# Kernel optimization log

Measured on AMD Instinct MI355X. Metric: run time of the kernel, lower is better.

The kernel has to match this reference:

```python
import jax, jax.numpy as jnp
import numpy as np

H = 32

def setup_inputs() -> dict:
    key = jax.random.key(0)
    ks = jax.random.split(key, 8)
    B, S = 256, 4096
    scale = 1.0 / np.sqrt(H)
    return {
        "lstm_outputs": jax.random.normal(ks[0], (B, S, H), dtype=jnp.float32),
        "final_hidden": jax.random.normal(ks[1], (B, H), dtype=jnp.float32),
        "Wq": jax.random.uniform(ks[2], (H, H), jnp.float32, -scale, scale),
        "bq": jax.random.uniform(ks[3], (H,), jnp.float32, -scale, scale),
        "Wk": jax.random.uniform(ks[4], (H, H), jnp.float32, -scale, scale),
        "bk": jax.random.uniform(ks[5], (H,), jnp.float32, -scale, scale),
        "Wv": jax.random.uniform(ks[6], (H, 1), jnp.float32, -scale, scale),
        "bv": jax.random.uniform(ks[7], (1,), jnp.float32, -scale, scale),
    }

def reference(lstm_outputs, final_hidden, Wq, bq, Wk, bk, Wv, bv):
    # keys: [B,S,H], query: [B,H]
    keys = jnp.einsum('bsh,hd->bsd', lstm_outputs, Wk) + bk
    query = final_hidden @ Wq + bq
    tanhed = jnp.tanh(query[:, None, :] + keys)            # [B,S,H]
    scores = jnp.einsum('bsh,h->bs', tanhed, Wv[:, 0]) + bv[0]  # [B,S]
    att_weights = jax.nn.softmax(scores, axis=-1)          # [B,S]
    context = jnp.einsum('bs,bsh->bh', att_weights, keys)  # [B,H]
    return context, att_weights
```

## Files before the change

### kernel.cpp

```cpp
#include <hip/hip_runtime.h>
#include <math.h>

#define HD 32
#define BB 256
#define SS 4096
#define BLK 256
#define POSB 256
#define NCH (SS / POSB)
#define PAD 33
#define PSTRIDE 33

__device__ __forceinline__ float tanh_fast(float x) {
  float e = __builtin_amdgcn_exp2f(x * 2.8853900817779268f);
  return 1.0f - 2.0f * __builtin_amdgcn_rcpf(e + 1.0f);
}
__device__ __forceinline__ float exp_fast(float x) {
  return __builtin_amdgcn_exp2f(x * 1.4426950408889634f);
}

__global__ void __launch_bounds__(BLK, 4) bahdanau_p1(
    const float* __restrict__ lstm, const float* __restrict__ fh,
    const float* __restrict__ Wq, const float* __restrict__ bq,
    const float* __restrict__ Wk, const float* __restrict__ bk,
    const float* __restrict__ Wv, const float* __restrict__ bv,
    float* __restrict__ scores_out, float* __restrict__ partials) {
  __shared__ float sX[POSB * PAD];
  __shared__ float sWk[HD * HD];
  __shared__ float sE[POSB];
  __shared__ float sQB[HD];
  __shared__ float sWv[HD];
  __shared__ float sYp[8][HD];
  __shared__ float sRedL[BLK / 64];

  const int tid = threadIdx.x;
  const int b = blockIdx.x >> 4;
  const int chunk = blockIdx.x & (NCH - 1);
  const int base = chunk * POSB;
  const int lane = tid & 63, wid = tid >> 6;

  ((float4*)sWk)[tid] = ((const float4*)Wk)[tid];

  const float* gx = lstm + ((size_t)b * SS + base) * HD;
  float4 stg[8];
#pragma unroll
  for (int i = 0; i < 8; i++) stg[i] = ((const float4*)gx)[tid + i * BLK];

  if (tid < HD) {
    float acc = bq[tid] + bk[tid];
    const float* fhb = fh + b * HD;
#pragma unroll
    for (int j = 0; j < HD; j++) acc += fhb[j] * Wq[j * HD + tid];
    sQB[tid] = acc;
    sWv[tid] = Wv[tid];
  }

#pragma unroll
  for (int i = 0; i < 8; i++) {
    const int f = tid + i * BLK;
    const int pos = f >> 3, q = f & 7;
    float* d = &sX[pos * PAD + q * 4];
    d[0] = stg[i].x; d[1] = stg[i].y; d[2] = stg[i].z; d[3] = stg[i].w;
  }
  __syncthreads();

  const float* xr = &sX[tid * PAD];
  float acc[HD];
#pragma unroll
  for (int h = 0; h < HD; h++) acc[h] = 0.f;
#pragma unroll 2
  for (int j = 0; j < HD; j++) {
    const float xj = xr[j];
    const float4* wrow = (const float4*)&sWk[j * HD];
#pragma unroll
    for (int h4 = 0; h4 < 8; h4++) {
      const float4 w = wrow[h4];
      acc[4 * h4 + 0] = fmaf(xj, w.x, acc[4 * h4 + 0]);
      acc[4 * h4 + 1] = fmaf(xj, w.y, acc[4 * h4 + 1]);
      acc[4 * h4 + 2] = fmaf(xj, w.z, acc[4 * h4 + 2]);
      acc[4 * h4 + 3] = fmaf(xj, w.w, acc[4 * h4 + 3]);
    }
  }

  float sc = bv[0];
#pragma unroll
  for (int h4 = 0; h4 < 8; h4++) {
    const float4 qb = ((const float4*)sQB)[h4];
    const float4 wv = ((const float4*)sWv)[h4];
    sc = fmaf(tanh_fast(qb.x + acc[4 * h4 + 0]), wv.x, sc);
    sc = fmaf(tanh_fast(qb.y + acc[4 * h4 + 1]), wv.y, sc);
    sc = fmaf(tanh_fast(qb.z + acc[4 * h4 + 2]), wv.z, sc);
    sc = fmaf(tanh_fast(qb.w + acc[4 * h4 + 3]), wv.w, sc);
  }
  const float e = exp_fast(sc);
  scores_out[(size_t)b * SS + base + tid] = e;
  sE[tid] = e;

  float lv = e;
#pragma unroll
  for (int off = 32; off >= 1; off >>= 1) lv += __shfl_xor(lv, off, 64);
  if (lane == 0) sRedL[wid] = lv;
  __syncthreads();

  const int j = tid & 31, g = tid >> 5;
  float cp = 0.f;
#pragma unroll
  for (int p = 0; p < 32; p++) {
    const int pos = g * 32 + p;
    cp = fmaf(sE[pos], sX[pos * PAD + j], cp);
  }
  sYp[g][j] = cp;
  __syncthreads();

  if (tid < HD) {
    float y = 0.f;
#pragma unroll
    for (int gg = 0; gg < 8; gg++) y += sYp[gg][tid];
    float* p = partials + (size_t)blockIdx.x * PSTRIDE;
    p[1 + tid] = y;
    if (tid == 0) p[0] = sRedL[0] + sRedL[1] + sRedL[2] + sRedL[3];
  }
}

__global__ void __launch_bounds__(BLK) bahdanau_p2(
    const float* __restrict__ partials, const float* __restrict__ Wk,
    const float* __restrict__ bk, float* __restrict__ ctx_out,
    float* __restrict__ scores) {
  const int blk = blockIdx.x;
  const int b = blk >> 2;
  const int tid = threadIdx.x;
  __shared__ float sY[HD];

  float L = 0.f;
#pragma unroll
  for (int c = 0; c < NCH; c++)
    L += partials[(size_t)(b * NCH + c) * PSTRIDE];
  const float invL = __builtin_amdgcn_rcpf(L);

  if ((blk & 3) == 0) {
    if (tid < HD) {
      float y = 0.f;
#pragma unroll
      for (int c = 0; c < NCH; c++)
        y += partials[(size_t)(b * NCH + c) * PSTRIDE + 1 + tid];
      sY[tid] = y;
    }
    __syncthreads();
    if (tid < HD) {
      float c = bk[tid] * L;
#pragma unroll
      for (int j = 0; j < HD; j++) c = fmaf(sY[j], Wk[j * HD + tid], c);
      ctx_out[b * HD + tid] = c * invL;
    }
  }

  float4* srow = (float4*)(scores + (size_t)b * SS + (blk & 3) * 1024);
  float4 s = srow[tid];
  s.x *= invL; s.y *= invL; s.z *= invL; s.w *= invL;
  srow[tid] = s;
}

extern "C" void kernel_launch(void* const* d_in, const int* in_sizes, int n_in,
                              void* d_out, int out_size, void* d_ws,
                              size_t ws_size, hipStream_t stream) {
  const float* lstm = (const float*)d_in[0];
  const float* fh   = (const float*)d_in[1];
  const float* Wq   = (const float*)d_in[2];
  const float* bq   = (const float*)d_in[3];
  const float* Wk   = (const float*)d_in[4];
  const float* bk   = (const float*)d_in[5];
  const float* Wv   = (const float*)d_in[6];
  const float* bv   = (const float*)d_in[7];

  float* out = (float*)d_out;
  float* ctx_out = out;
  float* scores = out + BB * HD;
  float* partials = (float*)d_ws;

  bahdanau_p1<<<BB * NCH, BLK, 0, stream>>>(lstm, fh, Wq, bq, Wk, bk, Wv, bv,
                                            scores, partials);
  bahdanau_p2<<<BB * 4, BLK, 0, stream>>>(partials, Wk, bk, ctx_out, scores);
}
```

Baseline: 210.4 us.

## Compute key projection with split-bf16 MFMA and drop LDS staging of inputs

Replaces the per-thread FP32 FMA projection of lstm rows by Wk with 16x16x32 bf16 MFMA instructions. Both operands are split into high and low bf16 parts and three MFMAs are summed to approximate FP32 accuracy. Each wave now loads its 64 rows straight from global into registers instead of staging the tile in shared memory. Score reduction, exp, and the weighted context accumulation are done with cross-lane shuffles. This cuts ALU and LDS work but adds shuffle overhead and a small loss of precision from the three-term bf16 split.

```diff
diff --git a/kernel.cpp b/kernel.cpp
--- a/kernel.cpp
+++ b/kernel.cpp
@@ -7,8 +7,11 @@
 #define BLK 256
 #define POSB 256
 #define NCH (SS / POSB)
-#define PAD 33
+#define PADW 40
 #define PSTRIDE 33
+
+typedef short bf16x8 __attribute__((ext_vector_type(8)));
+typedef float f32x4 __attribute__((ext_vector_type(4)));
 
 __device__ __forceinline__ float tanh_fast(float x) {
   float e = __builtin_amdgcn_exp2f(x * 2.8853900817779268f);
@@ -16,6 +19,12 @@
 }
 __device__ __forceinline__ float exp_fast(float x) {
   return __builtin_amdgcn_exp2f(x * 1.4426950408889634f);
+}
+__device__ __forceinline__ short bf16_trunc(float x) {
+  return (short)(__float_as_uint(x) >> 16);
+}
+__device__ __forceinline__ float hi_part(float x) {
+  return __uint_as_float(__float_as_uint(x) & 0xffff0000u);
 }
 
 __global__ void __launch_bounds__(BLK, 4) bahdanau_p1(
@@ -24,27 +33,31 @@
     const float* __restrict__ Wk, const float* __restrict__ bk,
     const float* __restrict__ Wv, const float* __restrict__ bv,
     float* __restrict__ scores_out, float* __restrict__ partials) {
-  __shared__ float sX[POSB * PAD];
-  __shared__ float sWk[HD * HD];
-  __shared__ float sE[POSB];
+  __shared__ short sWkTh[HD * PADW];
+  __shared__ short sWkTl[HD * PADW];
   __shared__ float sQB[HD];
   __shared__ float sWv[HD];
-  __shared__ float sYp[8][HD];
-  __shared__ float sRedL[BLK / 64];
+  __shared__ float sYp[4][HD];
+  __shared__ float sRedL[4];
 
   const int tid = threadIdx.x;
   const int b = blockIdx.x >> 4;
   const int chunk = blockIdx.x & (NCH - 1);
   const int base = chunk * POSB;
-  const int lane = tid & 63, wid = tid >> 6;
-
-  ((float4*)sWk)[tid] = ((const float4*)Wk)[tid];
-
-  const float* gx = lstm + ((size_t)b * SS + base) * HD;
-  float4 stg[8];
-#pragma unroll
-  for (int i = 0; i < 8; i++) stg[i] = ((const float4*)gx)[tid + i * BLK];
-
+  const int lane = tid & 63, w = tid >> 6;
+  const int col = lane & 15, quad = lane >> 4;
+
+  {
+    float4 w4 = ((const float4*)Wk)[tid];
+    const int k = tid >> 3, h0 = (tid & 7) * 4;
+    const float v[4] = {w4.x, w4.y, w4.z, w4.w};
+#pragma unroll
+    for (int i = 0; i < 4; i++) {
+      const float hf = hi_part(v[i]);
+      sWkTh[(h0 + i) * PADW + k] = bf16_trunc(v[i]);
+      sWkTl[(h0 + i) * PADW + k] = bf16_trunc(v[i] - hf);
+    }
+  }
   if (tid < HD) {
     float acc = bq[tid] + bk[tid];
     const float* fhb = fh + b * HD;
@@ -53,68 +66,85 @@
     sQB[tid] = acc;
     sWv[tid] = Wv[tid];
   }
-
-#pragma unroll
-  for (int i = 0; i < 8; i++) {
-    const int f = tid + i * BLK;
-    const int pos = f >> 3, q = f & 7;
-    float* d = &sX[pos * PAD + q * 4];
-    d[0] = stg[i].x; d[1] = stg[i].y; d[2] = stg[i].z; d[3] = stg[i].w;
-  }
   __syncthreads();
 
-  const float* xr = &sX[tid * PAD];
-  float acc[HD];
-#pragma unroll
-  for (int h = 0; h < HD; h++) acc[h] = 0.f;
-#pragma unroll 2
-  for (int j = 0; j < HD; j++) {
-    const float xj = xr[j];
-    const float4* wrow = (const float4*)&sWk[j * HD];
-#pragma unroll
-    for (int h4 = 0; h4 < 8; h4++) {
-      const float4 w = wrow[h4];
-      acc[4 * h4 + 0] = fmaf(xj, w.x, acc[4 * h4 + 0]);
-      acc[4 * h4 + 1] = fmaf(xj, w.y, acc[4 * h4 + 1]);
-      acc[4 * h4 + 2] = fmaf(xj, w.z, acc[4 * h4 + 2]);
-      acc[4 * h4 + 3] = fmaf(xj, w.w, acc[4 * h4 + 3]);
-    }
-  }
-
-  float sc = bv[0];
-#pragma unroll
-  for (int h4 = 0; h4 < 8; h4++) {
-    const float4 qb = ((const float4*)sQB)[h4];
-    const float4 wv = ((const float4*)sWv)[h4];
-    sc = fmaf(tanh_fast(qb.x + acc[4 * h4 + 0]), wv.x, sc);
-    sc = fmaf(tanh_fast(qb.y + acc[4 * h4 + 1]), wv.y, sc);
-    sc = fmaf(tanh_fast(qb.z + acc[4 * h4 + 2]), wv.z, sc);
-    sc = fmaf(tanh_fast(qb.w + acc[4 * h4 + 3]), wv.w, sc);
-  }
-  const float e = exp_fast(sc);
-  scores_out[(size_t)b * SS + base + tid] = e;
-  sE[tid] = e;
-
-  float lv = e;
-#pragma unroll
-  for (int off = 32; off >= 1; off >>= 1) lv += __shfl_xor(lv, off, 64);
-  if (lane == 0) sRedL[wid] = lv;
+  bf16x8 Bh0 = *(const bf16x8*)&sWkTh[(col) * PADW + quad * 8];
+  bf16x8 Bl0 = *(const bf16x8*)&sWkTl[(col) * PADW + quad * 8];
+  bf16x8 Bh1 = *(const bf16x8*)&sWkTh[(16 + col) * PADW + quad * 8];
+  bf16x8 Bl1 = *(const bf16x8*)&sWkTl[(16 + col) * PADW + quad * 8];
+  const float qb0 = sQB[col], qb1 = sQB[16 + col];
+  const float wv0 = sWv[col], wv1 = sWv[16 + col];
+  const float bv0 = bv[0];
+
+  const float* gx = lstm + ((size_t)b * SS + base + w * 64) * HD;
+  float lAcc = 0.f;
+  float yp[8];
+#pragma unroll
+  for (int j = 0; j < 8; j++) yp[j] = 0.f;
+
+#pragma unroll
+  for (int mt = 0; mt < 4; mt++) {
+    const float* rp = gx + (size_t)(mt * 16 + col) * HD + quad * 8;
+    const float4 xa = ((const float4*)rp)[0];
+    const float4 xb = ((const float4*)rp)[1];
+    const float xs[8] = {xa.x, xa.y, xa.z, xa.w, xb.x, xb.y, xb.z, xb.w};
+    bf16x8 Ah, Al;
+#pragma unroll
+    for (int j = 0; j < 8; j++) {
+      const float hf = hi_part(xs[j]);
+      Ah[j] = bf16_trunc(xs[j]);
+      Al[j] = bf16_trunc(xs[j] - hf);
+    }
+    f32x4 c0 = {0.f, 0.f, 0.f, 0.f}, c1 = {0.f, 0.f, 0.f, 0.f};
+    c0 = __builtin_amdgcn_mfma_f32_16x16x32_bf16(Ah, Bh0, c0, 0, 0, 0);
+    c0 = __builtin_amdgcn_mfma_f32_16x16x32_bf16(Al, Bh0, c0, 0, 0, 0);
+    c0 = __builtin_amdgcn_mfma_f32_16x16x32_bf16(Ah, Bl0, c0, 0, 0, 0);
+    c1 = __builtin_amdgcn_mfma_f32_16x16x32_bf16(Ah, Bh1, c1, 0, 0, 0);
+    c1 = __builtin_amdgcn_mfma_f32_16x16x32_bf16(Al, Bh1, c1, 0, 0, 0);
+    c1 = __builtin_amdgcn_mfma_f32_16x16x32_bf16(Ah, Bl1, c1, 0, 0, 0);
+
+    float esc[4];
+#pragma unroll
+    for (int r = 0; r < 4; r++) {
+      float t = tanh_fast(qb0 + c0[r]) * wv0 + tanh_fast(qb1 + c1[r]) * wv1;
+      t += __shfl_xor(t, 1, 64);
+      t += __shfl_xor(t, 2, 64);
+      t += __shfl_xor(t, 4, 64);
+      t += __shfl_xor(t, 8, 64);
+      esc[r] = exp_fast(t + bv0);
+    }
+    const int srcLane = (col >> 2) * 16;
+    const float g0 = __shfl(esc[0], srcLane, 64);
+    const float g1 = __shfl(esc[1], srcLane, 64);
+    const float g2 = __shfl(esc[2], srcLane, 64);
+    const float g3 = __shfl(esc[3], srcLane, 64);
+    const int rr = col & 3;
+    const float e_m = (rr == 0) ? g0 : (rr == 1) ? g1 : (rr == 2) ? g2 : g3;
+    if (lane < 16)
+      scores_out[(size_t)b * SS + base + w * 64 + mt * 16 + lane] = e_m;
+    lAcc += (lane < 16) ? e_m : 0.f;
+#pragma unroll
+    for (int j = 0; j < 8; j++) yp[j] = fmaf(e_m, xs[j], yp[j]);
+  }
+
+#pragma unroll
+  for (int j = 0; j < 8; j++) {
+    yp[j] += __shfl_xor(yp[j], 1, 64);
+    yp[j] += __shfl_xor(yp[j], 2, 64);
+    yp[j] += __shfl_xor(yp[j], 4, 64);
+    yp[j] += __shfl_xor(yp[j], 8, 64);
+  }
+  if (col == 0) {
+#pragma unroll
+    for (int j = 0; j < 8; j++) sYp[w][quad * 8 + j] = yp[j];
+  }
+#pragma unroll
+  for (int off = 32; off >= 1; off >>= 1) lAcc += __shfl_xor(lAcc, off, 64);
+  if (lane == 0) sRedL[w] = lAcc;
   __syncthreads();
 
-  const int j = tid & 31, g = tid >> 5;
-  float cp = 0.f;
-#pragma unroll
-  for (int p = 0; p < 32; p++) {
-    const int pos = g * 32 + p;
-    cp = fmaf(sE[pos], sX[pos * PAD + j], cp);
-  }
-  sYp[g][j] = cp;
-  __syncthreads();
-
   if (tid < HD) {
-    float y = 0.f;
-#pragma unroll
-    for (int gg = 0; gg < 8; gg++) y += sYp[gg][tid];
+    float y = sYp[0][tid] + sYp[1][tid] + sYp[2][tid] + sYp[3][tid];
     float* p = partials + (size_t)blockIdx.x * PSTRIDE;
     p[1 + tid] = y;
     if (tid == 0) p[0] = sRedL[0] + sRedL[1] + sRedL[2] + sRedL[3];
```

Result: no change. 212.0 us (+0.7%).
